# Optimization experiments

Hardware: AMD Instinct MI355X
Metric: run time of the kernel (lower is better)

The kernel has to match this reference:

```python
import jax, jax.numpy as jnp
import numpy as np

B, N, D, H, DA, DL = 8, 1024, 512, 8, 64, 64
U_DIM = DL * H * 3          # 1536: u channel (3 attention channels worth)
NB = 128                    # timestamp-delta buckets
HID = 4 * D                 # FFN hidden (ffn_multiply=4)
EPS = 1e-6


def _rms(x):
    return x * jax.lax.rsqrt(jnp.mean(x * x, axis=-1, keepdims=True) + EPS)


def setup_inputs() -> dict:
    key = jax.random.key(0)
    ks = jax.random.split(key, 12)
    L = N // 2
    total = B * L
    x_offsets = jnp.arange(B + 1, dtype=jnp.int32) * L
    x = jax.random.normal(ks[0], (total, D), jnp.float32)
    all_timestamps = jnp.sort(jax.random.randint(ks[1], (B, N), 0, 1_000_000, dtype=jnp.int64), axis=1)
    invalid_attn_mask = jnp.tril(jnp.ones((N, N), jnp.float32))
    uvqk = jax.random.normal(ks[2], (D, DL * H * 4 + DA * H * 2), jnp.float32) * 0.02
    pos_w = jax.random.normal(ks[3], (2 * N - 1,), jnp.float32) * 0.02
    ts_w = jax.random.normal(ks[4], (NB,), jnp.float32) * 0.02
    W0 = jax.random.normal(ks[5], (U_DIM, D), jnp.float32) * (1.0 / np.sqrt(U_DIM))
    b0 = jnp.zeros((D,), jnp.float32)
    W1 = jax.random.normal(ks[6], (D, HID), jnp.float32) * (1.0 / np.sqrt(D))
    W2 = jax.random.normal(ks[7], (HID, D), jnp.float32) * (1.0 / np.sqrt(HID))
    W3 = jax.random.normal(ks[8], (D, HID), jnp.float32) * (1.0 / np.sqrt(D))
    return dict(x=x, x_offsets=x_offsets, all_timestamps=all_timestamps,
                invalid_attn_mask=invalid_attn_mask, uvqk=uvqk, pos_w=pos_w,
                ts_w=ts_w, W0=W0, b0=b0, W1=W1, W2=W2, W3=W3)


def reference(x, x_offsets, all_timestamps, invalid_attn_mask, uvqk, pos_w, ts_w, W0, b0, W1, W2, W3):
    total = x.shape[0]
    tok = jnp.arange(total)
    b_idx = jnp.searchsorted(x_offsets, tok, side='right') - 1   # batch id per jagged token
    p_idx = tok - x_offsets[b_idx]                               # position within sequence

    # input RMSNorm + fused uvqk projection with SiLU
    normed = _rms(x)
    mm = jax.nn.silu(normed @ uvqk)
    u, v, q, k = jnp.split(mm, [U_DIM, U_DIM + DL * H, U_DIM + DL * H + DA * H], axis=1)

    def pad(vals):  # jagged_to_padded_dense
        return jnp.zeros((B, N, vals.shape[-1]), vals.dtype).at[b_idx, p_idx].set(vals)

    pq = pad(q).reshape(B, N, H, DA)
    pk = pad(k).reshape(B, N, H, DA)
    pv = pad(v).reshape(B, N, H, DL)

    # channel 1: content-content SiLU attention
    qk_attn = jax.nn.silu(jnp.einsum('bnhd,bmhd->bhnm', pq, pk)) / N
    qk_attn = qk_attn * invalid_attn_mask[None, None]

    # channel 2: relative positional bias (shared across batch)
    rel = jnp.arange(N)[:, None] - jnp.arange(N)[None, :] + (N - 1)
    pos_attn = pos_w[rel] * invalid_attn_mask                     # (N, N)

    # channel 3: log-bucketed relative temporal bias
    dt = all_timestamps[:, :, None] - all_timestamps[:, None, :]
    bucket = jnp.clip(jnp.floor(jnp.log(jnp.abs(dt).astype(jnp.float32) + 1.0)).astype(jnp.int32), 0, NB - 1)
    ts_attn = ts_w[bucket] * invalid_attn_mask[None]              # (B, N, N)

    out_pos = jnp.einsum('nm,bmhd->bnhd', pos_attn, pv)
    out_ts = jnp.einsum('bnm,bmhd->bnhd', ts_attn, pv)
    out_lat = jnp.einsum('bhnm,bmhd->bnhd', qk_attn, pv)
    combined = jnp.concatenate([out_pos, out_ts, out_lat], axis=-1).reshape(B, N, U_DIM)
    attn_output = combined[b_idx, p_idx]                          # dense_to_jagged

    # AMS gating + multistage FFN with residuals
    ams = u * _rms(attn_output)
    X = ams @ W0 + b0 + x
    nX = _rms(X)
    X1 = jax.nn.silu(nX @ W1) * (nX @ W3)
    return X1 @ W2 + X
```

## Files before the change

kernel.cpp:

```cpp
#include <hip/hip_runtime.h>
#include <hip/hip_bf16.h>
#include <cstdint>
#include <cstddef>

typedef __hip_bfloat16 bf16;
typedef __attribute__((ext_vector_type(8))) short bf8v;
typedef __attribute__((ext_vector_type(4))) float f4v;
typedef __attribute__((ext_vector_type(4))) short s4v;
typedef __attribute__((ext_vector_type(8))) short s8v;

#define DEV static __device__ __forceinline__

DEV float siluf(float v){ return v / (1.0f + __expf(-v)); }
DEV short bfs(float f){ bf16 h = __float2bfloat16(f); return __builtin_bit_cast(short, h); }
DEV float b2f(short s){ return __builtin_bit_cast(float, (unsigned)((unsigned short)s) << 16); }

DEV void gload16(const bf16* g, bf16* l){
  __builtin_amdgcn_global_load_lds((const __attribute__((address_space(1))) void*)g,
                                   (__attribute__((address_space(3))) void*)l, 16, 0, 0);
}

template<int BN>
DEV void gemm_core(const bf16* __restrict__ A, int lda,
                   const bf16* __restrict__ Bt, int ldb,
                   int K, bf16* As, bf16* Bs, f4v (&acc)[4][4],
                   int bm, int bn, int k0)
{
  constexpr int NT = (BN==128)?256:128;
  const int t = threadIdx.x, w = t>>6, l = t&63;
  const int wr = (BN==128)?(w>>1):w;
  const int wc = (BN==128)?(w&1):0;
  const int lr = l&15, kb = l>>4;
#pragma unroll
  for (int i=0;i<4;i++)
#pragma unroll
    for (int j=0;j<4;j++) acc[i][j] = (f4v)(0.0f);

  for (int kt=k0; kt<k0+K; kt+=32){
    __syncthreads();
#pragma unroll
    for (int i=0;i<512/NT;i++){
      int lin = t + i*NT;
      gload16(A + (size_t)(bm + (lin>>2))*lda + kt + (lin&3)*8,
              As + (size_t)(w*64 + i*NT)*8);
    }
#pragma unroll
    for (int i=0;i<(BN*4)/NT;i++){
      int lin = t + i*NT;
      gload16(Bt + (size_t)(bn + (lin>>2))*ldb + kt + (lin&3)*8,
              Bs + (size_t)(w*64 + i*NT)*8);
    }
    __syncthreads();
    bf8v af[4], bfr[4];
#pragma unroll
    for (int i=0;i<4;i++) af[i]  = *(const bf8v*)(As + (wr*64 + i*16 + lr)*32 + kb*8);
#pragma unroll
    for (int j=0;j<4;j++) bfr[j] = *(const bf8v*)(Bs + (wc*64 + j*16 + lr)*32 + kb*8);
#pragma unroll
    for (int i=0;i<4;i++)
#pragma unroll
      for (int j=0;j<4;j++)
        acc[i][j] = __builtin_amdgcn_mfma_f32_16x16x32_bf16(af[i], bfr[j], acc[i][j], 0,0,0);
  }
}

#define EPI_LOOP(BN, ...) { \
  const int t_=threadIdx.x, w_=t_>>6, l_=t_&63; \
  const int wr_=(BN==128)?(w_>>1):w_, wc_=(BN==128)?(w_&1):0; \
  const int lr_=l_&15, kb_=l_>>4; \
  _Pragma("unroll") for (int i_=0;i_<4;i_++) \
  _Pragma("unroll") for (int j_=0;j_<4;j_++) \
  _Pragma("unroll") for (int r_=0;r_<4;r_++){ \
    const int row = bm + wr_*64 + i_*16 + kb_*4 + r_; \
    const int col = bn + wc_*64 + j_*16 + lr_; \
    float v = acc[i_][j_][r_]; \
    __VA_ARGS__; \
  } }


__global__ __launch_bounds__(256) void k_gemm1(const bf16* __restrict__ xn,
                                               const bf16* __restrict__ uvqkT,
                                               bf16* __restrict__ mm,
                                               bf16* __restrict__ vT){
  __shared__ __align__(16) bf16 As[128*32];
  __shared__ __align__(16) bf16 Bs[128*32];
  f4v acc[4][4];
  const int bm = blockIdx.x*128, bn = blockIdx.y*128;
  gemm_core<128>(xn, 512, uvqkT, 512, 512, As, Bs, acc, bm, bn, 0);
  const int t=threadIdx.x, w=t>>6, l=t&63;
  const int wr=w>>1, wc=w&1, lr=l&15, kb=l>>4;
  const bool isv = (bn >= 1536) && (bn < 2048);
#pragma unroll
  for (int i=0;i<4;i++)
#pragma unroll
  for (int j=0;j<4;j++){
    const int row0 = bm + wr*64 + i*16 + kb*4;
    const int col  = bn + wc*64 + j*16 + lr;
    if (!isv){
#pragma unroll
      for (int r=0;r<4;r++)
        mm[(size_t)(row0+r)*3072 + col] = __float2bfloat16(siluf(acc[i][j][r]));
    } else {
      s4v p;
#pragma unroll
      for (int r=0;r<4;r++) p[r] = bfs(siluf(acc[i][j][r]));
      const int b = row0 >> 9, m = row0 & 511;
      *(s4v*)(vT + ((size_t)b*512 + (col-1536))*512 + m) = p;
    }
  }
}

__global__ __launch_bounds__(256) void k_attn_lat(const bf16* __restrict__ mm,
                                                  const bf16* __restrict__ vT,
                                                  bf16* __restrict__ comb){
  __shared__ __align__(16) bf16 Qs[2*128*32];
  __shared__ __align__(16) bf16 Ks[2*128*32];
  __shared__ __align__(16) bf16 Vs[4*64*32];
  __shared__ __align__(16) bf16 Ss[4*128*32];
  const int bm = blockIdx.x*128;
  const int z = blockIdx.y, b = z>>3, h = z&7;
  const int t = threadIdx.x, w = t>>6, l = t&63;
  const int wr = w>>1, wc = w&1, lr = l&15, kb = l>>4;
  const bf16* Qg = mm + (size_t)b*512*3072 + 2048 + h*64;
  const bf16* Kg = mm + (size_t)b*512*3072 + 2560 + h*64;
  const bf16* Vg = vT + ((size_t)b*512 + h*64)*512;
  f4v o[4][2];
#pragma unroll
  for (int i=0;i<4;i++)
#pragma unroll
    for (int j=0;j<2;j++) o[i][j] = (f4v)(0.0f);

#pragma unroll
  for (int p=0;p<4;p++){
    int s = t + p*256;
    gload16(Qg + (size_t)(bm + ((s>>2)&127))*3072 + (s>>9)*32 + (s&3)*8,
            Qs + (size_t)(w*64 + p*256)*8);
  }
  for (int bn=0; bn<=bm; bn+=128){
    __syncthreads();
#pragma unroll
    for (int p=0;p<4;p++){
      int s = t + p*256;
      gload16(Kg + (size_t)(bn + ((s>>2)&127))*3072 + (s>>9)*32 + (s&3)*8,
              Ks + (size_t)(w*64 + p*256)*8);
    }
#pragma unroll
    for (int p=0;p<4;p++){
      int s = t + p*256;
      gload16(Vg + (size_t)((s>>2)&63)*512 + bn + (s>>8)*32 + (s&3)*8,
              Vs + (size_t)(w*64 + p*256)*8);
    }
    __syncthreads();
    f4v sacc[4][4];
#pragma unroll
    for (int i=0;i<4;i++)
#pragma unroll
      for (int j=0;j<4;j++) sacc[i][j] = (f4v)(0.0f);
#pragma unroll
    for (int ki=0; ki<2; ki++){
      bf8v af[4], bk[4];
#pragma unroll
      for (int i=0;i<4;i++) af[i] = *(const bf8v*)(Qs + ki*4096 + (wr*64+i*16+lr)*32 + kb*8);
#pragma unroll
      for (int j=0;j<4;j++) bk[j] = *(const bf8v*)(Ks + ki*4096 + (wc*64+j*16+lr)*32 + kb*8);
#pragma unroll
      for (int i=0;i<4;i++)
#pragma unroll
        for (int j=0;j<4;j++)
          sacc[i][j] = __builtin_amdgcn_mfma_f32_16x16x32_bf16(af[i], bk[j], sacc[i][j], 0,0,0);
    }
    const bool diag = (bn == bm);
#pragma unroll
    for (int i=0;i<4;i++)
#pragma unroll
    for (int j=0;j<4;j++)
#pragma unroll
    for (int r=0;r<4;r++){
      const int row = wr*64 + i*16 + kb*4 + r;
      const int col = wc*64 + j*16 + lr;
      float sv = siluf(sacc[i][j][r])*(1.0f/1024.0f);
      if (diag && row < col) sv = 0.0f;
      Ss[(col>>5)*4096 + row*32 + (col&31)] = __float2bfloat16(sv);
    }
    __syncthreads();
#pragma unroll
    for (int kt=0; kt<4; kt++){
      bf8v af[4], bv[2];
#pragma unroll
      for (int i=0;i<4;i++) af[i] = *(const bf8v*)(Ss + kt*4096 + (wr*64+i*16+lr)*32 + kb*8);
#pragma unroll
      for (int j=0;j<2;j++) bv[j] = *(const bf8v*)(Vs + kt*2048 + (wc*32+j*16+lr)*32 + kb*8);
#pragma unroll
      for (int i=0;i<4;i++)
#pragma unroll
        for (int j=0;j<2;j++)
          o[i][j] = __builtin_amdgcn_mfma_f32_16x16x32_bf16(af[i], bv[j], o[i][j], 0,0,0);
    }
  }
#pragma unroll
  for (int i=0;i<4;i++)
#pragma unroll
  for (int j=0;j<2;j++)
#pragma unroll
  for (int r=0;r<4;r++){
    const int row = bm + wr*64 + i*16 + kb*4 + r;
    const int col = wc*32 + j*16 + lr;
    comb[((size_t)b*512 + row)*1536 + h*192 + 128 + col] = __float2bfloat16(o[i][j][r]);
  }
}

__global__ __launch_bounds__(256) void k_pv_posts(const bf16* __restrict__ Apos,
                                                  const bf16* __restrict__ Ats,
                                                  const bf16* __restrict__ vT,
                                                  bf16* __restrict__ comb){
  __shared__ __align__(16) bf16 As[128*32];
  __shared__ __align__(16) bf16 Bs[128*32];
  f4v acc[4][4];
  const int z = blockIdx.z, b = z>>1, ch = z&1;
  const bf16* A  = ch ? (Ats + (size_t)b*512*512) : Apos;
  const bf16* Bt = vT + (size_t)b*512*512;
  const int bm = blockIdx.x*128, bn = blockIdx.y*128;
  gemm_core<128>(A, 512, Bt, 512, bm + 128, As, Bs, acc, bm, bn, 0);
  EPI_LOOP(128, comb[((size_t)b*512 + row)*1536 + (col>>6)*192 + ch*64 + (col&63)]
                    = __float2bfloat16(v); )
}

__global__ __launch_bounds__(256) void k_gemm_w0_sk(const bf16* __restrict__ ams,
                                                    const bf16* __restrict__ W0T,
                                                    float* __restrict__ parts){
  __shared__ __align__(16) bf16 As[128*32];
  __shared__ __align__(16) bf16 Bs[128*32];
  f4v acc[4][4];
  const int bm = blockIdx.x*128, bn = blockIdx.y*128, k0 = blockIdx.z*384;
  gemm_core<128>(ams, 1536, W0T, 1536, 384, As, Bs, acc, bm, bn, k0);
  float* P = parts + (size_t)blockIdx.z*4096*512;
  EPI_LOOP(128, P[(size_t)row*512 + col] = v; )
}

__global__ __launch_bounds__(128) void k_reduce_w0_rms(const float* __restrict__ parts,
                                                       const float* __restrict__ x,
                                                       const float* __restrict__ b0,
                                                       float* __restrict__ X,
                                                       bf16* __restrict__ nX){
  __shared__ float sbuf[16];
  const size_t row = blockIdx.x;
  const int t = threadIdx.x;
  float4 s = ((const float4*)(x + row*512))[t];
  const float4 bv = ((const float4*)b0)[t];
  s.x += bv.x; s.y += bv.y; s.z += bv.z; s.w += bv.w;
#pragma unroll
  for (int p=0;p<4;p++){
    const float4 pv = ((const float4*)(parts + (size_t)p*4096*512 + row*512))[t];
    s.x += pv.x; s.y += pv.y; s.z += pv.z; s.w += pv.w;
  }
  ((float4*)(X + row*512))[t] = s;
  float ss = s.x*s.x + s.y*s.y + s.z*s.z + s.w*s.w;
#pragma unroll
  for (int o=32;o>0;o>>=1) ss += __shfl_down(ss, o);
  const int ln = t & 63, wv = t >> 6;
  if (ln==0) sbuf[wv] = ss;
  __syncthreads();
  if (t==0) sbuf[8] = rsqrtf((sbuf[0]+sbuf[1])*(1.0f/512.0f) + 1e-6f);
  __syncthreads();
  const float r = sbuf[8];
  s4v o; o[0]=bfs(s.x*r); o[1]=bfs(s.y*r); o[2]=bfs(s.z*r); o[3]=bfs(s.w*r);
  ((s4v*)(nX + row*512))[t] = o;
}

__global__ __launch_bounds__(256) void k_gemm_w13f(const bf16* __restrict__ nX,
                                                   const bf16* __restrict__ W1T,
                                                   const bf16* __restrict__ W3T,
                                                   bf16* __restrict__ X1){
  __shared__ __align__(16) bf16 As[128*32];
  __shared__ __align__(16) bf16 Bs1[64*32];
  __shared__ __align__(16) bf16 Bs3[64*32];
  f4v a1[4][2], a3[4][2];
  const int bm = blockIdx.x*128, bn = blockIdx.y*64;
  const int t = threadIdx.x, w = t>>6, l = t&63;
  const int wr = w>>1, wc = w&1, lr = l&15, kb = l>>4;
#pragma unroll
  for (int i=0;i<4;i++)
#pragma unroll
    for (int j=0;j<2;j++){ a1[i][j] = (f4v)(0.0f); a3[i][j] = (f4v)(0.0f); }

  for (int kt=0; kt<512; kt+=32){
    __syncthreads();
#pragma unroll
    for (int i=0;i<2;i++){
      int lin = t + i*256;
      gload16(nX + (size_t)(bm + (lin>>2))*512 + kt + (lin&3)*8, As + (size_t)(w*64 + i*256)*8);
    }
    gload16(W1T + (size_t)(bn + (t>>2))*512 + kt + (t&3)*8, Bs1 + (size_t)(w*64)*8);
    gload16(W3T + (size_t)(bn + (t>>2))*512 + kt + (t&3)*8, Bs3 + (size_t)(w*64)*8);
    __syncthreads();
    bf8v af[4], b1[2], b3[2];
#pragma unroll
    for (int i=0;i<4;i++) af[i] = *(const bf8v*)(As + (wr*64 + i*16 + lr)*32 + kb*8);
#pragma unroll
    for (int j=0;j<2;j++){ b1[j] = *(const bf8v*)(Bs1 + (wc*32 + j*16 + lr)*32 + kb*8);
                           b3[j] = *(const bf8v*)(Bs3 + (wc*32 + j*16 + lr)*32 + kb*8); }
#pragma unroll
    for (int i=0;i<4;i++)
#pragma unroll
      for (int j=0;j<2;j++){
        a1[i][j] = __builtin_amdgcn_mfma_f32_16x16x32_bf16(af[i], b1[j], a1[i][j], 0,0,0);
        a3[i][j] = __builtin_amdgcn_mfma_f32_16x16x32_bf16(af[i], b3[j], a3[i][j], 0,0,0);
      }
  }
#pragma unroll
  for (int i=0;i<4;i++)
#pragma unroll
  for (int j=0;j<2;j++)
#pragma unroll
  for (int r=0;r<4;r++){
    const int row = bm + wr*64 + i*16 + kb*4 + r;
    const int col = bn + wc*32 + j*16 + lr;
    X1[(size_t)row*2048 + col] = __float2bfloat16(siluf(a1[i][j][r]) * a3[i][j][r]);
  }
}

__global__ __launch_bounds__(256) void k_gemm_w2_sk(const bf16* __restrict__ X1,
                                                    const bf16* __restrict__ W2T,
                                                    float* __restrict__ parts){
  __shared__ __align__(16) bf16 As[128*32];
  __shared__ __align__(16) bf16 Bs[128*32];
  f4v acc[4][4];
  const int bm = blockIdx.x*128, bn = blockIdx.y*128, k0 = blockIdx.z*512;
  gemm_core<128>(X1, 2048, W2T, 2048, 512, As, Bs, acc, bm, bn, k0);
  float* P = parts + (size_t)blockIdx.z*4096*512;
  EPI_LOOP(128, P[(size_t)row*512 + col] = v; )
}

__global__ __launch_bounds__(256) void k_reduce_w2(const float* __restrict__ parts,
                                                   float* __restrict__ out){
  const int i = blockIdx.x*256 + threadIdx.x;
  float4 s = ((const float4*)out)[i];
#pragma unroll
  for (int p=0;p<4;p++){
    const float4 pv = ((const float4*)(parts + (size_t)p*4096*512))[i];
    s.x += pv.x; s.y += pv.y; s.z += pv.z; s.w += pv.w;
  }
  ((float4*)out)[i] = s;
}


__global__ __launch_bounds__(192) void k_rms_mul_u(const bf16* __restrict__ comb,
                                                   const bf16* __restrict__ mm,
                                                   bf16* __restrict__ ams){
  __shared__ float sbuf[16];
  const size_t rb = (size_t)blockIdx.x;
  const s8v cv = ((const s8v*)(comb + rb*1536))[threadIdx.x];
  float cf[8]; float ss = 0.f;
#pragma unroll
  for (int j=0;j<8;j++){ cf[j] = b2f(cv[j]); ss += cf[j]*cf[j]; }
#pragma unroll
  for (int o=32;o>0;o>>=1) ss += __shfl_down(ss, o);
  const int ln = threadIdx.x & 63, wv = threadIdx.x >> 6;
  if (ln==0) sbuf[wv] = ss;
  __syncthreads();
  if (threadIdx.x==0) sbuf[8] = rsqrtf((sbuf[0]+sbuf[1]+sbuf[2])*(1.0f/1536.0f) + 1e-6f);
  __syncthreads();
  const float r = sbuf[8];
  const s8v uv = ((const s8v*)(mm + rb*3072))[threadIdx.x];
  s8v o;
#pragma unroll
  for (int j=0;j<8;j++) o[j] = bfs(b2f(uv[j]) * cf[j] * r);
  ((s8v*)(ams + rb*1536))[threadIdx.x] = o;
}

__global__ __launch_bounds__(256) void k_prep(
    const float* __restrict__ x,    const int* __restrict__ ts,
    const float* __restrict__ pos_w,const float* __restrict__ ts_w,
    const float* __restrict__ uvqk, const float* __restrict__ W0,
    const float* __restrict__ W1,   const float* __restrict__ W3,
    const float* __restrict__ W2,
    bf16* __restrict__ xn,
    bf16* __restrict__ uvqkT, bf16* __restrict__ W0T,
    bf16* __restrict__ W13T,  bf16* __restrict__ W2T,
    bf16* __restrict__ Apos,  bf16* __restrict__ Ats){
  __shared__ float tile[32][33];
  __shared__ float sbuf[16];
  int id = blockIdx.x;
  if (id < 5376){
    const float* src; bf16* dst; int R, C;
    if      (id < 1536){            src=uvqk; dst=uvqkT;                  R=512;  C=3072; }
    else if (id < 2304){ id-=1536;  src=W0;   dst=W0T;                    R=1536; C=512;  }
    else if (id < 3328){ id-=2304;  src=W1;   dst=W13T;                   R=512;  C=2048; }
    else if (id < 4352){ id-=3328;  src=W3;   dst=W13T+(size_t)2048*512;  R=512;  C=2048; }
    else               { id-=4352;  src=W2;   dst=W2T;                    R=2048; C=512;  }
    const int nbx = C >> 5;
    const int c0 = (id % nbx)*32, r0 = (id / nbx)*32;
    const int tx = threadIdx.x & 31, ty = threadIdx.x >> 5;
#pragma unroll
    for (int i=0;i<32;i+=8) tile[ty+i][tx] = src[(size_t)(r0+ty+i)*C + (c0+tx)];
    __syncthreads();
#pragma unroll
    for (int i=0;i<32;i+=8) dst[(size_t)(c0+ty+i)*R + (r0+tx)] = __float2bfloat16(tile[tx][ty+i]);
  } else if (id < 14592){
    int id2 = id - 5376;
    const int mblk = id2 & 1, n = (id2>>1)&511, z = id2>>10;
    if (mblk*256 > n) return;
    const int m = mblk*256 + threadIdx.x;
    if (z == 0){
      float v = (n >= m) ? pos_w[n - m + 1023] : 0.f;
      Apos[(size_t)n*512 + m] = __float2bfloat16(v);
    } else {
      const int b = z-1;
      int dt = ts[b*1024 + n] - ts[b*1024 + m];
      float ad = (float)(dt < 0 ? -dt : dt);
      int bucket = (int)floorf(logf(ad + 1.0f));
      bucket = bucket < 0 ? 0 : (bucket > 127 ? 127 : bucket);
      float v = (n >= m) ? ts_w[bucket] : 0.f;
      Ats[((size_t)b*512 + n)*512 + m] = __float2bfloat16(v);
    }
  } else {
    const size_t row = id - 14592;
    const int t = threadIdx.x;
    if (t >= 128) return;
    const float4 v = ((const float4*)(x + row*512))[t];
    float ss = v.x*v.x + v.y*v.y + v.z*v.z + v.w*v.w;
#pragma unroll
    for (int o=32;o>0;o>>=1) ss += __shfl_down(ss, o);
    const int ln = t & 63, wv = t >> 6;
    if (ln==0) sbuf[wv] = ss;
    __syncthreads();
    if (t==0) sbuf[8] = rsqrtf((sbuf[0]+sbuf[1])*(1.0f/512.0f) + 1e-6f);
    __syncthreads();
    const float r = sbuf[8];
    s4v o; o[0]=bfs(v.x*r); o[1]=bfs(v.y*r); o[2]=bfs(v.z*r); o[3]=bfs(v.w*r);
    ((s4v*)(xn + row*512))[t] = o;
  }
}


extern "C" void kernel_launch(void* const* d_in, const int* in_sizes, int n_in,
                              void* d_out, int out_size, void* d_ws, size_t ws_size,
                              hipStream_t stream) {
  const float* x     = (const float*)d_in[0];
  const int*   ts    = (const int*)d_in[2];
  const float* uvqk  = (const float*)d_in[4];
  const float* pos_w = (const float*)d_in[5];
  const float* ts_w  = (const float*)d_in[6];
  const float* W0    = (const float*)d_in[7];
  const float* b0    = (const float*)d_in[8];
  const float* W1    = (const float*)d_in[9];
  const float* W2    = (const float*)d_in[10];
  const float* W3    = (const float*)d_in[11];
  float* out = (float*)d_out;

  char* w = (char*)d_ws;
  auto alloc = [&](size_t bytes){ char* p = w; w += (bytes + 255) & ~(size_t)255; return p; };
  bf16*  xn    = (bf16*)alloc((size_t)4096*512*2);
  bf16*  uvqkT = (bf16*)alloc((size_t)3072*512*2);
  bf16*  W0T   = (bf16*)alloc((size_t)512*1536*2);
  bf16*  W13T  = (bf16*)alloc((size_t)4096*512*2);
  bf16*  W2T   = (bf16*)alloc((size_t)512*2048*2);
  bf16*  mm    = (bf16*)alloc((size_t)4096*3072*2);
  bf16*  vT    = (bf16*)alloc((size_t)8*512*512*2);
  bf16*  Apos  = (bf16*)alloc((size_t)512*512*2);
  bf16*  Ats   = (bf16*)alloc((size_t)8*512*512*2);
  bf16*  X1    = (bf16*)alloc((size_t)4096*2048*2);
  bf16*  comb  = (bf16*)alloc((size_t)4096*1536*2);
  bf16*  ams   = (bf16*)alloc((size_t)4096*1536*2);
  bf16*  nX    = (bf16*)alloc((size_t)4096*512*2);
  float* parts = (float*)alloc((size_t)4*4096*512*4);

  k_prep<<<18688, 256, 0, stream>>>(x, ts, pos_w, ts_w, uvqk, W0, W1, W3, W2,
                                    xn, uvqkT, W0T, W13T, W2T, Apos, Ats);
  k_gemm1<<<dim3(32, 24), 256, 0, stream>>>(xn, uvqkT, mm, vT);
  k_attn_lat<<<dim3(4, 64), 256, 0, stream>>>(mm, vT, comb);
  k_pv_posts<<<dim3(4, 4, 16), 256, 0, stream>>>(Apos, Ats, vT, comb);
  k_rms_mul_u<<<4096, 192, 0, stream>>>(comb, mm, ams);
  k_gemm_w0_sk<<<dim3(32, 4, 4), 256, 0, stream>>>(ams, W0T, parts);
  k_reduce_w0_rms<<<4096, 128, 0, stream>>>(parts, x, b0, out, nX);
  k_gemm_w13f<<<dim3(32, 32), 256, 0, stream>>>(nX, W13T, W13T + (size_t)2048*512, X1);
  k_gemm_w2_sk<<<dim3(32, 4, 4), 256, 0, stream>>>(X1, W2T, parts);
  k_reduce_w2<<<2048, 256, 0, stream>>>(parts, out);
}
```

Measured before the change: 169.5 us.

## Double K-step per barrier in GEMMs and merge attention kernels into one launch

Every bf16 GEMM core, including the fused W1/W3 kernel, now loads a 64-wide K slab (two 32-wide sub-tiles) between each pair of barriers. This halves the number of __syncthreads per tile but doubles the LDS footprint. The latent-attention kernel and the positional/timestamp PV kernel are merged into a single 512-block launch that branches on block id and shares one LDS buffer. The merge removes a launch and lets both kinds of work run concurrently, at the cost of a larger shared-memory allocation that may reduce occupancy for the GEMM blocks.

```diff
diff --git a/kernel.cpp b/kernel.cpp
--- a/kernel.cpp
+++ b/kernel.cpp
@@ -20,54 +20,55 @@
                                    (__attribute__((address_space(3))) void*)l, 16, 0, 0);
 }
 
-template<int BN>
-DEV void gemm_core(const bf16* __restrict__ A, int lda,
-                   const bf16* __restrict__ Bt, int ldb,
-                   int K, bf16* As, bf16* Bs, f4v (&acc)[4][4],
-                   int bm, int bn, int k0)
+DEV void gemm_core128(const bf16* __restrict__ A, int lda,
+                      const bf16* __restrict__ Bt, int ldb,
+                      int K, bf16* As, bf16* Bs, f4v (&acc)[4][4],
+                      int bm, int bn, int k0)
 {
-  constexpr int NT = (BN==128)?256:128;
   const int t = threadIdx.x, w = t>>6, l = t&63;
-  const int wr = (BN==128)?(w>>1):w;
-  const int wc = (BN==128)?(w&1):0;
-  const int lr = l&15, kb = l>>4;
+  const int wr = w>>1, wc = w&1, lr = l&15, kb = l>>4;
 #pragma unroll
   for (int i=0;i<4;i++)
 #pragma unroll
     for (int j=0;j<4;j++) acc[i][j] = (f4v)(0.0f);
 
-  for (int kt=k0; kt<k0+K; kt+=32){
-    __syncthreads();
-#pragma unroll
-    for (int i=0;i<512/NT;i++){
-      int lin = t + i*NT;
-      gload16(A + (size_t)(bm + (lin>>2))*lda + kt + (lin&3)*8,
-              As + (size_t)(w*64 + i*NT)*8);
-    }
-#pragma unroll
-    for (int i=0;i<(BN*4)/NT;i++){
-      int lin = t + i*NT;
-      gload16(Bt + (size_t)(bn + (lin>>2))*ldb + kt + (lin&3)*8,
-              Bs + (size_t)(w*64 + i*NT)*8);
-    }
-    __syncthreads();
-    bf8v af[4], bfr[4];
-#pragma unroll
-    for (int i=0;i<4;i++) af[i]  = *(const bf8v*)(As + (wr*64 + i*16 + lr)*32 + kb*8);
-#pragma unroll
-    for (int j=0;j<4;j++) bfr[j] = *(const bf8v*)(Bs + (wc*64 + j*16 + lr)*32 + kb*8);
-#pragma unroll
-    for (int i=0;i<4;i++)
-#pragma unroll
-      for (int j=0;j<4;j++)
-        acc[i][j] = __builtin_amdgcn_mfma_f32_16x16x32_bf16(af[i], bfr[j], acc[i][j], 0,0,0);
-  }
-}
-
-#define EPI_LOOP(BN, ...) { \
+  for (int kt=k0; kt<k0+K; kt+=64){
+    __syncthreads();
+#pragma unroll
+    for (int s=0;s<2;s++){
+#pragma unroll
+      for (int i=0;i<2;i++){
+        int lin = t + i*256;
+        gload16(A + (size_t)(bm + (lin>>2))*lda + kt + s*32 + (lin&3)*8,
+                As + s*4096 + (size_t)(w*64 + i*256)*8);
+      }
+#pragma unroll
+      for (int i=0;i<2;i++){
+        int lin = t + i*256;
+        gload16(Bt + (size_t)(bn + (lin>>2))*ldb + kt + s*32 + (lin&3)*8,
+                Bs + s*4096 + (size_t)(w*64 + i*256)*8);
+      }
+    }
+    __syncthreads();
+#pragma unroll
+    for (int s=0;s<2;s++){
+      bf8v af[4], bfr[4];
+#pragma unroll
+      for (int i=0;i<4;i++) af[i]  = *(const bf8v*)(As + s*4096 + (wr*64 + i*16 + lr)*32 + kb*8);
+#pragma unroll
+      for (int j=0;j<4;j++) bfr[j] = *(const bf8v*)(Bs + s*4096 + (wc*64 + j*16 + lr)*32 + kb*8);
+#pragma unroll
+      for (int i=0;i<4;i++)
+#pragma unroll
+        for (int j=0;j<4;j++)
+          acc[i][j] = __builtin_amdgcn_mfma_f32_16x16x32_bf16(af[i], bfr[j], acc[i][j], 0,0,0);
+    }
+  }
+}
+
+#define EPI_LOOP(...) { \
   const int t_=threadIdx.x, w_=t_>>6, l_=t_&63; \
-  const int wr_=(BN==128)?(w_>>1):w_, wc_=(BN==128)?(w_&1):0; \
-  const int lr_=l_&15, kb_=l_>>4; \
+  const int wr_=w_>>1, wc_=w_&1, lr_=l_&15, kb_=l_>>4; \
   _Pragma("unroll") for (int i_=0;i_<4;i_++) \
   _Pragma("unroll") for (int j_=0;j_<4;j_++) \
   _Pragma("unroll") for (int r_=0;r_<4;r_++){ \
@@ -82,11 +83,11 @@
                                                const bf16* __restrict__ uvqkT,
                                                bf16* __restrict__ mm,
                                                bf16* __restrict__ vT){
-  __shared__ __align__(16) bf16 As[128*32];
-  __shared__ __align__(16) bf16 Bs[128*32];
+  __shared__ __align__(16) bf16 As[2*128*32];
+  __shared__ __align__(16) bf16 Bs[2*128*32];
   f4v acc[4][4];
   const int bm = blockIdx.x*128, bn = blockIdx.y*128;
-  gemm_core<128>(xn, 512, uvqkT, 512, 512, As, Bs, acc, bm, bn, 0);
+  gemm_core128(xn, 512, uvqkT, 512, 512, As, Bs, acc, bm, bn, 0);
   const int t=threadIdx.x, w=t>>6, l=t&63;
   const int wr=w>>1, wc=w&1, lr=l&15, kb=l>>4;
   const bool isv = (bn >= 1536) && (bn < 2048);
@@ -110,131 +111,134 @@
   }
 }
 
-__global__ __launch_bounds__(256) void k_attn_lat(const bf16* __restrict__ mm,
-                                                  const bf16* __restrict__ vT,
-                                                  bf16* __restrict__ comb){
-  __shared__ __align__(16) bf16 Qs[2*128*32];
-  __shared__ __align__(16) bf16 Ks[2*128*32];
-  __shared__ __align__(16) bf16 Vs[4*64*32];
-  __shared__ __align__(16) bf16 Ss[4*128*32];
-  const int bm = blockIdx.x*128;
-  const int z = blockIdx.y, b = z>>3, h = z&7;
+__global__ __launch_bounds__(256) void k_attn(const bf16* __restrict__ mm,
+                                              const bf16* __restrict__ vT,
+                                              const bf16* __restrict__ Apos,
+                                              const bf16* __restrict__ Ats,
+                                              bf16* __restrict__ comb){
+  __shared__ __align__(16) bf16 smem[40960];
+  const int id = blockIdx.x;
   const int t = threadIdx.x, w = t>>6, l = t&63;
   const int wr = w>>1, wc = w&1, lr = l&15, kb = l>>4;
-  const bf16* Qg = mm + (size_t)b*512*3072 + 2048 + h*64;
-  const bf16* Kg = mm + (size_t)b*512*3072 + 2560 + h*64;
-  const bf16* Vg = vT + ((size_t)b*512 + h*64)*512;
-  f4v o[4][2];
-#pragma unroll
-  for (int i=0;i<4;i++)
-#pragma unroll
-    for (int j=0;j<2;j++) o[i][j] = (f4v)(0.0f);
-
-#pragma unroll
-  for (int p=0;p<4;p++){
-    int s = t + p*256;
-    gload16(Qg + (size_t)(bm + ((s>>2)&127))*3072 + (s>>9)*32 + (s&3)*8,
-            Qs + (size_t)(w*64 + p*256)*8);
-  }
-  for (int bn=0; bn<=bm; bn+=128){
-    __syncthreads();
+
+  if (id < 256){
+    bf16* Qs = smem;
+    bf16* Ks = smem + 8192;
+    bf16* Vs = smem + 16384;
+    bf16* Ss = smem + 24576;
+    const int bm = (id & 3)*128;
+    const int z = id >> 2, b = z>>3, h = z&7;
+    const bf16* Qg = mm + (size_t)b*512*3072 + 2048 + h*64;
+    const bf16* Kg = mm + (size_t)b*512*3072 + 2560 + h*64;
+    const bf16* Vg = vT + ((size_t)b*512 + h*64)*512;
+    f4v o[4][2];
+#pragma unroll
+    for (int i=0;i<4;i++)
+#pragma unroll
+      for (int j=0;j<2;j++) o[i][j] = (f4v)(0.0f);
+
 #pragma unroll
     for (int p=0;p<4;p++){
       int s = t + p*256;
-      gload16(Kg + (size_t)(bn + ((s>>2)&127))*3072 + (s>>9)*32 + (s&3)*8,
-              Ks + (size_t)(w*64 + p*256)*8);
-    }
-#pragma unroll
-    for (int p=0;p<4;p++){
-      int s = t + p*256;
-      gload16(Vg + (size_t)((s>>2)&63)*512 + bn + (s>>8)*32 + (s&3)*8,
-              Vs + (size_t)(w*64 + p*256)*8);
-    }
-    __syncthreads();
-    f4v sacc[4][4];
+      gload16(Qg + (size_t)(bm + ((s>>2)&127))*3072 + (s>>9)*32 + (s&3)*8,
+              Qs + (size_t)(w*64 + p*256)*8);
+    }
+    for (int bn=0; bn<=bm; bn+=128){
+      __syncthreads();
+#pragma unroll
+      for (int p=0;p<4;p++){
+        int s = t + p*256;
+        gload16(Kg + (size_t)(bn + ((s>>2)&127))*3072 + (s>>9)*32 + (s&3)*8,
+                Ks + (size_t)(w*64 + p*256)*8);
+      }
+#pragma unroll
+      for (int p=0;p<4;p++){
+        int s = t + p*256;
+        gload16(Vg + (size_t)((s>>2)&63)*512 + bn + (s>>8)*32 + (s&3)*8,
+                Vs + (size_t)(w*64 + p*256)*8);
+      }
+      __syncthreads();
+      f4v sacc[4][4];
+#pragma unroll
+      for (int i=0;i<4;i++)
+#pragma unroll
+        for (int j=0;j<4;j++) sacc[i][j] = (f4v)(0.0f);
+#pragma unroll
+      for (int ki=0; ki<2; ki++){
+        bf8v af[4], bk[4];
+#pragma unroll
+        for (int i=0;i<4;i++) af[i] = *(const bf8v*)(Qs + ki*4096 + (wr*64+i*16+lr)*32 + kb*8);
+#pragma unroll
+        for (int j=0;j<4;j++) bk[j] = *(const bf8v*)(Ks + ki*4096 + (wc*64+j*16+lr)*32 + kb*8);
+#pragma unroll
+        for (int i=0;i<4;i++)
+#pragma unroll
+          for (int j=0;j<4;j++)
+            sacc[i][j] = __builtin_amdgcn_mfma_f32_16x16x32_bf16(af[i], bk[j], sacc[i][j], 0,0,0);
+      }
+      const bool diag = (bn == bm);
+#pragma unroll
+      for (int i=0;i<4;i++)
+#pragma unroll
+      for (int j=0;j<4;j++)
+#pragma unroll
+      for (int r=0;r<4;r++){
+        const int row = wr*64 + i*16 + kb*4 + r;
+        const int col = wc*64 + j*16 + lr;
+        float sv = siluf(sacc[i][j][r])*(1.0f/1024.0f);
+        if (diag && row < col) sv = 0.0f;
+        Ss[(col>>5)*4096 + row*32 + (col&31)] = __float2bfloat16(sv);
+      }
+      __syncthreads();
+#pragma unroll
+      for (int kt=0; kt<4; kt++){
+        bf8v af[4], bv[2];
+#pragma unroll
+        for (int i=0;i<4;i++) af[i] = *(const bf8v*)(Ss + kt*4096 + (wr*64+i*16+lr)*32 + kb*8);
+#pragma unroll
+        for (int j=0;j<2;j++) bv[j] = *(const bf8v*)(Vs + kt*2048 + (wc*32+j*16+lr)*32 + kb*8);
+#pragma unroll
+        for (int i=0;i<4;i++)
+#pragma unroll
+          for (int j=0;j<2;j++)
+            o[i][j] = __builtin_amdgcn_mfma_f32_16x16x32_bf16(af[i], bv[j], o[i][j], 0,0,0);
+      }
+    }
 #pragma unroll
     for (int i=0;i<4;i++)
 #pragma unroll
-      for (int j=0;j<4;j++) sacc[i][j] = (f4v)(0.0f);
-#pragma unroll
-    for (int ki=0; ki<2; ki++){
-      bf8v af[4], bk[4];
-#pragma unroll
-      for (int i=0;i<4;i++) af[i] = *(const bf8v*)(Qs + ki*4096 + (wr*64+i*16+lr)*32 + kb*8);
-#pragma unroll
-      for (int j=0;j<4;j++) bk[j] = *(const bf8v*)(Ks + ki*4096 + (wc*64+j*16+lr)*32 + kb*8);
-#pragma unroll
-      for (int i=0;i<4;i++)
-#pragma unroll
-        for (int j=0;j<4;j++)
-          sacc[i][j] = __builtin_amdgcn_mfma_f32_16x16x32_bf16(af[i], bk[j], sacc[i][j], 0,0,0);
-    }
-    const bool diag = (bn == bm);
-#pragma unroll
-    for (int i=0;i<4;i++)
-#pragma unroll
-    for (int j=0;j<4;j++)
+    for (int j=0;j<2;j++)
 #pragma unroll
     for (int r=0;r<4;r++){
-      const int row = wr*64 + i*16 + kb*4 + r;
-      const int col = wc*64 + j*16 + lr;
-      float sv = siluf(sacc[i][j][r])*(1.0f/1024.0f);
-      if (diag && row < col) sv = 0.0f;
-      Ss[(col>>5)*4096 + row*32 + (col&31)] = __float2bfloat16(sv);
-    }
-    __syncthreads();
-#pragma unroll
-    for (int kt=0; kt<4; kt++){
-      bf8v af[4], bv[2];
-#pragma unroll
-      for (int i=0;i<4;i++) af[i] = *(const bf8v*)(Ss + kt*4096 + (wr*64+i*16+lr)*32 + kb*8);
-#pragma unroll
-      for (int j=0;j<2;j++) bv[j] = *(const bf8v*)(Vs + kt*2048 + (wc*32+j*16+lr)*32 + kb*8);
-#pragma unroll
-      for (int i=0;i<4;i++)
-#pragma unroll
-        for (int j=0;j<2;j++)
-          o[i][j] = __builtin_amdgcn_mfma_f32_16x16x32_bf16(af[i], bv[j], o[i][j], 0,0,0);
-    }
-  }
-#pragma unroll
-  for (int i=0;i<4;i++)
-#pragma unroll
-  for (int j=0;j<2;j++)
-#pragma unroll
-  for (int r=0;r<4;r++){
-    const int row = bm + wr*64 + i*16 + kb*4 + r;
-    const int col = wc*32 + j*16 + lr;
-    comb[((size_t)b*512 + row)*1536 + h*192 + 128 + col] = __float2bfloat16(o[i][j][r]);
-  }
-}
-
-__global__ __launch_bounds__(256) void k_pv_posts(const bf16* __restrict__ Apos,
-                                                  const bf16* __restrict__ Ats,
-                                                  const bf16* __restrict__ vT,
-                                                  bf16* __restrict__ comb){
-  __shared__ __align__(16) bf16 As[128*32];
-  __shared__ __align__(16) bf16 Bs[128*32];
-  f4v acc[4][4];
-  const int z = blockIdx.z, b = z>>1, ch = z&1;
-  const bf16* A  = ch ? (Ats + (size_t)b*512*512) : Apos;
-  const bf16* Bt = vT + (size_t)b*512*512;
-  const int bm = blockIdx.x*128, bn = blockIdx.y*128;
-  gemm_core<128>(A, 512, Bt, 512, bm + 128, As, Bs, acc, bm, bn, 0);
-  EPI_LOOP(128, comb[((size_t)b*512 + row)*1536 + (col>>6)*192 + ch*64 + (col&63)]
-                    = __float2bfloat16(v); )
+      const int row = bm + wr*64 + i*16 + kb*4 + r;
+      const int col = wc*32 + j*16 + lr;
+      comb[((size_t)b*512 + row)*1536 + h*192 + 128 + col] = __float2bfloat16(o[i][j][r]);
+    }
+  } else {
+    bf16* As = smem;
+    bf16* Bs = smem + 8192;
+    f4v acc[4][4];
+    const int id2 = id - 256;
+    const int bm = (id2 & 3)*128, bn = ((id2>>2)&3)*128;
+    const int z = id2 >> 4, b = z>>1, ch = z&1;
+    const bf16* A  = ch ? (Ats + (size_t)b*512*512) : Apos;
+    const bf16* Bt = vT + (size_t)b*512*512;
+    gemm_core128(A, 512, Bt, 512, bm + 128, As, Bs, acc, bm, bn, 0);
+    EPI_LOOP( comb[((size_t)b*512 + row)*1536 + (col>>6)*192 + ch*64 + (col&63)]
+                  = __float2bfloat16(v); )
+  }
 }
 
 __global__ __launch_bounds__(256) void k_gemm_w0_sk(const bf16* __restrict__ ams,
                                                     const bf16* __restrict__ W0T,
                                                     float* __restrict__ parts){
-  __shared__ __align__(16) bf16 As[128*32];
-  __shared__ __align__(16) bf16 Bs[128*32];
+  __shared__ __align__(16) bf16 As[2*128*32];
+  __shared__ __align__(16) bf16 Bs[2*128*32];
   f4v acc[4][4];
   const int bm = blockIdx.x*128, bn = blockIdx.y*128, k0 = blockIdx.z*384;
-  gemm_core<128>(ams, 1536, W0T, 1536, 384, As, Bs, acc, bm, bn, k0);
+  gemm_core128(ams, 1536, W0T, 1536, 384, As, Bs, acc, bm, bn, k0);
   float* P = parts + (size_t)blockIdx.z*4096*512;
-  EPI_LOOP(128, P[(size_t)row*512 + col] = v; )
+  EPI_LOOP( P[(size_t)row*512 + col] = v; )
 }
 
 __global__ __launch_bounds__(128) void k_reduce_w0_rms(const float* __restrict__ parts,
@@ -271,9 +275,9 @@
                                                    const bf16* __restrict__ W1T,
                                                    const bf16* __restrict__ W3T,
                                                    bf16* __restrict__ X1){
-  __shared__ __align__(16) bf16 As[128*32];
-  __shared__ __align__(16) bf16 Bs1[64*32];
-  __shared__ __align__(16) bf16 Bs3[64*32];
+  __shared__ __align__(16) bf16 As[2*128*32];
+  __shared__ __align__(16) bf16 Bs1[2*64*32];
+  __shared__ __align__(16) bf16 Bs3[2*64*32];
   f4v a1[4][2], a3[4][2];
   const int bm = blockIdx.x*128, bn = blockIdx.y*64;
   const int t = threadIdx.x, w = t>>6, l = t&63;
@@ -283,29 +287,36 @@
 #pragma unroll
     for (int j=0;j<2;j++){ a1[i][j] = (f4v)(0.0f); a3[i][j] = (f4v)(0.0f); }
 
-  for (int kt=0; kt<512; kt+=32){
-    __syncthreads();
-#pragma unroll
-    for (int i=0;i<2;i++){
-      int lin = t + i*256;
-      gload16(nX + (size_t)(bm + (lin>>2))*512 + kt + (lin&3)*8, As + (size_t)(w*64 + i*256)*8);
-    }
-    gload16(W1T + (size_t)(bn + (t>>2))*512 + kt + (t&3)*8, Bs1 + (size_t)(w*64)*8);
-    gload16(W3T + (size_t)(bn + (t>>2))*512 + kt + (t&3)*8, Bs3 + (size_t)(w*64)*8);
-    __syncthreads();
-    bf8v af[4], b1[2], b3[2];
-#pragma unroll
-    for (int i=0;i<4;i++) af[i] = *(const bf8v*)(As + (wr*64 + i*16 + lr)*32 + kb*8);
-#pragma unroll
-    for (int j=0;j<2;j++){ b1[j] = *(const bf8v*)(Bs1 + (wc*32 + j*16 + lr)*32 + kb*8);
-                           b3[j] = *(const bf8v*)(Bs3 + (wc*32 + j*16 + lr)*32 + kb*8); }
-#pragma unroll
-    for (int i=0;i<4;i++)
-#pragma unroll
-      for (int j=0;j<2;j++){
-        a1[i][j] = __builtin_amdgcn_mfma_f32_16x16x32_bf16(af[i], b1[j], a1[i][j], 0,0,0);
-        a3[i][j] = __builtin_amdgcn_mfma_f32_16x16x32_bf16(af[i], b3[j], a3[i][j], 0,0,0);
-      }
+  for (int kt=0; kt<512; kt+=64){
+    __syncthreads();
+#pragma unroll
+    for (int s=0;s<2;s++){
+#pragma unroll
+      for (int i=0;i<2;i++){
+        int lin = t + i*256;
+        gload16(nX + (size_t)(bm + (lin>>2))*512 + kt + s*32 + (lin&3)*8,
+                As + s*4096 + (size_t)(w*64 + i*256)*8);
+      }
+      gload16(W1T + (size_t)(bn + (t>>2))*512 + kt + s*32 + (t&3)*8, Bs1 + s*2048 + (size_t)(w*64)*8);
+      gload16(W3T + (size_t)(bn + (t>>2))*512 + kt + s*32 + (t&3)*8, Bs3 + s*2048 + (size_t)(w*64)*8);
+    }
+    __syncthreads();
+#pragma unroll
+    for (int s=0;s<2;s++){
+      bf8v af[4], b1[2], b3[2];
+#pragma unroll
+      for (int i=0;i<4;i++) af[i] = *(const bf8v*)(As + s*4096 + (wr*64 + i*16 + lr)*32 + kb*8);
+#pragma unroll
+      for (int j=0;j<2;j++){ b1[j] = *(const bf8v*)(Bs1 + s*2048 + (wc*32 + j*16 + lr)*32 + kb*8);
+                             b3[j] = *(const bf8v*)(Bs3 + s*2048 + (wc*32 + j*16 + lr)*32 + kb*8); }
+#pragma unroll
+      for (int i=0;i<4;i++)
+#pragma unroll
+        for (int j=0;j<2;j++){
+          a1[i][j] = __builtin_amdgcn_mfma_f32_16x16x32_bf16(af[i], b1[j], a1[i][j], 0,0,0);
+          a3[i][j] = __builtin_amdgcn_mfma_f32_16x16x32_bf16(af[i], b3[j], a3[i][j], 0,0,0);
+        }
+    }
   }
 #pragma unroll
   for (int i=0;i<4;i++)
@@ -322,13 +333,13 @@
 __global__ __launch_bounds__(256) void k_gemm_w2_sk(const bf16* __restrict__ X1,
                                                     const bf16* __restrict__ W2T,
                                                     float* __restrict__ parts){
-  __shared__ __align__(16) bf16 As[128*32];
-  __shared__ __align__(16) bf16 Bs[128*32];
+  __shared__ __align__(16) bf16 As[2*128*32];
+  __shared__ __align__(16) bf16 Bs[2*128*32];
   f4v acc[4][4];
   const int bm = blockIdx.x*128, bn = blockIdx.y*128, k0 = blockIdx.z*512;
-  gemm_core<128>(X1, 2048, W2T, 2048, 512, As, Bs, acc, bm, bn, k0);
+  gemm_core128(X1, 2048, W2T, 2048, 512, As, Bs, acc, bm, bn, k0);
   float* P = parts + (size_t)blockIdx.z*4096*512;
-  EPI_LOOP(128, P[(size_t)row*512 + col] = v; )
+  EPI_LOOP( P[(size_t)row*512 + col] = v; )
 }
 
 __global__ __launch_bounds__(256) void k_reduce_w2(const float* __restrict__ parts,
@@ -468,8 +479,7 @@
   k_prep<<<18688, 256, 0, stream>>>(x, ts, pos_w, ts_w, uvqk, W0, W1, W3, W2,
                                     xn, uvqkT, W0T, W13T, W2T, Apos, Ats);
   k_gemm1<<<dim3(32, 24), 256, 0, stream>>>(xn, uvqkT, mm, vT);
-  k_attn_lat<<<dim3(4, 64), 256, 0, stream>>>(mm, vT, comb);
-  k_pv_posts<<<dim3(4, 4, 16), 256, 0, stream>>>(Apos, Ats, vT, comb);
+  k_attn<<<512, 256, 0, stream>>>(mm, vT, Apos, Ats, comb);
   k_rms_mul_u<<<4096, 192, 0, stream>>>(comb, mm, ams);
   k_gemm_w0_sk<<<dim3(32, 4, 4), 256, 0, stream>>>(ams, W0T, parts);
   k_reduce_w0_rms<<<4096, 128, 0, stream>>>(parts, x, b0, out, nX);
```

Result: faster. 152.0 us (-10.3%).
